# Kernel optimization log

Hardware: AMD Instinct MI355X
Metric: run time of the kernel (lower is better)

The kernel has to match this reference:

```python
import jax, jax.numpy as jnp
import numpy as np


def setup_inputs() -> dict:
    key = jax.random.key(0)
    x = jax.random.normal(key, (8192, 4096), dtype=jnp.float32)
    return {"x": x, "p": 64}


def reference(x, p):
    # training-mode path: find top-p indices per row (descending sort, first p)
    # and overwrite those positions with -1000. mask = ones, so mask*x == x.
    _, idx = jax.lax.top_k(x, p)                      # [B, p] int32
    rows = jnp.arange(x.shape[0])[:, None]            # [B, 1]
    out = x.at[rows, idx].set(jnp.float32(-1000.0))
    return out
```

## Files before the change

kernel.cpp:

```cpp
#include <hip/hip_runtime.h>
#include <stdint.h>

#define COLS 4096
#define NEGV (-1000.0f)

__device__ __forceinline__ uint32_t f2key(float f) {
    uint32_t u = __float_as_uint(f);
    return u ^ (uint32_t)(((int32_t)u >> 31) | (int32_t)0x80000000);
}

extern "C" __global__ __launch_bounds__(256, 4)
void intent_dropout_kernel(const float* __restrict__ x,
                           const int* __restrict__ pp,
                           float* __restrict__ out) {
    __shared__ uint32_t s_keys[COLS];
    __shared__ float    s_grpmax[64];
    __shared__ float    s_C;
    __shared__ uint32_t s_cnt;
    __shared__ uint32_t s_Tkey;
    __shared__ uint32_t s_keq;
    __shared__ uint32_t s_eqcnt;
    __shared__ int      s_eqidx[256];

    const int row  = blockIdx.x;
    const int t    = threadIdx.x;
    const int lane = t & 63;
    const uint32_t P = (uint32_t)pp[0];

    const float4* xr = (const float4*)(x + (size_t)row * COLS);
    float4*       orow = (float4*)(out + (size_t)row * COLS);

    float4 v[4];
#pragma unroll
    for (int j = 0; j < 4; ++j) v[j] = xr[t + 256 * j];

    if (t == 0) { s_cnt = 0u; s_eqcnt = 0u; }

#pragma unroll
    for (int j = 0; j < 4; ++j) {
        float m = fmaxf(fmaxf(v[j].x, v[j].y), fmaxf(v[j].z, v[j].w));
#pragma unroll
        for (int d = 1; d < 16; d <<= 1) m = fmaxf(m, __shfl_xor(m, d, 64));
        if ((lane & 15) == 0) s_grpmax[(t >> 4) + 16 * j] = m;
    }
    __syncthreads();
    if (t < 64) {
        float g = s_grpmax[t];
#pragma unroll
        for (int d = 1; d < 64; d <<= 1) g = fminf(g, __shfl_xor(g, d, 64));
        if (t == 0) s_C = g;
    }
    __syncthreads();
    const uint32_t Ckey = f2key(s_C);

#define PUSH(F) do {                                                         \
        uint32_t k_ = f2key(F);                                              \
        bool pred_ = (k_ >= Ckey);                                           \
        unsigned long long m_ = __ballot(pred_);                             \
        if (m_) {                                                            \
            int ldr_ = (int)__builtin_ctzll(m_);                             \
            uint32_t base_ = 0u;                                             \
            if (lane == ldr_) base_ = atomicAdd(&s_cnt, (uint32_t)__popcll(m_)); \
            base_ = (uint32_t)__shfl((int)base_, ldr_, 64);                  \
            if (pred_) {                                                     \
                uint32_t off_ = (uint32_t)__popcll(m_ & ((1ull << lane) - 1ull)); \
                s_keys[base_ + off_] = k_;                                   \
            }                                                                \
        }                                                                    \
    } while (0)

#pragma unroll
    for (int j = 0; j < 4; ++j) {
        PUSH(v[j].x); PUSH(v[j].y); PUSH(v[j].z); PUSH(v[j].w);
    }
    __syncthreads();
    const uint32_t M = s_cnt;

    if (t < 64) {
        uint32_t rem = P, prefix = 0u;
        if (M <= 1024u) {
            uint32_t kk[16];
#pragma unroll
            for (int q = 0; q < 16; ++q) {
                uint32_t slot = (uint32_t)lane + 64u * q;
                kk[q] = (slot < M) ? s_keys[slot] : 0u;
            }
#pragma unroll
            for (int b = 31; b >= 0; --b) {
                uint32_t cand = prefix | (1u << b);
                uint32_t cnt = 0u;
#pragma unroll
                for (int q = 0; q < 16; ++q)
                    cnt += (uint32_t)(((kk[q] ^ cand) >> b) == 0u);
#pragma unroll
                for (int d = 1; d < 64; d <<= 1) cnt += __shfl_xor(cnt, d, 64);
                if (cnt >= rem) prefix = cand; else rem -= cnt;
            }
        } else {
            uint32_t nk = (M + 63u) >> 6;
            for (int b = 31; b >= 0; --b) {
                uint32_t cand = prefix | (1u << b);
                uint32_t cnt = 0u;
                for (uint32_t q = 0; q < nk; ++q) {
                    uint32_t slot = (uint32_t)lane + 64u * q;
                    if (slot < M)
                        cnt += (uint32_t)(((s_keys[slot] ^ cand) >> b) == 0u);
                }
#pragma unroll
                for (int d = 1; d < 64; d <<= 1) cnt += __shfl_xor(cnt, d, 64);
                if (cnt >= rem) prefix = cand; else rem -= cnt;
            }
        }
        if (t == 0) { s_Tkey = prefix; s_keq = rem; }
    }
    __syncthreads();
    const uint32_t Tkey = s_Tkey;
    const uint32_t keq  = s_keq;

#define EQPUSH(F, IDX) do {                                                  \
        if (f2key(F) == Tkey) {                                              \
            uint32_t s_ = atomicAdd(&s_eqcnt, 1u);                           \
            if (s_ < 256u) s_eqidx[s_] = (IDX);                              \
        }                                                                    \
    } while (0)

#pragma unroll
    for (int j = 0; j < 4; ++j) {
        EQPUSH(v[j].x, 4 * t + 1024 * j + 0);
        EQPUSH(v[j].y, 4 * t + 1024 * j + 1);
        EQPUSH(v[j].z, 4 * t + 1024 * j + 2);
        EQPUSH(v[j].w, 4 * t + 1024 * j + 3);
    }
    __syncthreads();
    const uint32_t eqc = s_eqcnt;

#define PROC(F, IDX) do {                                                    \
        uint32_t k_ = f2key(F);                                              \
        if (k_ > Tkey) { F = NEGV; }                                         \
        else if (k_ == Tkey) {                                               \
            int myi_ = (IDX);                                                \
            uint32_t r_ = 0u;                                                \
            uint32_t n_ = (eqc < 256u) ? eqc : 256u;                         \
            for (uint32_t e = 0; e < n_; ++e)                                \
                r_ += (uint32_t)(s_eqidx[e] < myi_);                         \
            if (r_ < keq) F = NEGV;                                          \
        }                                                                    \
    } while (0)

#pragma unroll
    for (int j = 0; j < 4; ++j) {
        float4 o = v[j];
        PROC(o.x, 4 * t + 1024 * j + 0);
        PROC(o.y, 4 * t + 1024 * j + 1);
        PROC(o.z, 4 * t + 1024 * j + 2);
        PROC(o.w, 4 * t + 1024 * j + 3);
        orow[t + 256 * j] = o;
    }
}

extern "C" void kernel_launch(void* const* d_in, const int* in_sizes, int n_in,
                              void* d_out, int out_size, void* d_ws, size_t ws_size,
                              hipStream_t stream) {
    const float* x  = (const float*)d_in[0];
    const int*   pp = (const int*)d_in[1];
    float*       out = (float*)d_out;
    int rows = in_sizes[0] / COLS;
    hipLaunchKernelGGL(intent_dropout_kernel, dim3(rows), dim3(256), 0, stream,
                       x, pp, out);
}
```

Measured before the change: 250.4 us.

## Replace single-wave bitwise radix select with block-wide 3-pass histogram select

Replaces the 32-iteration bitwise radix search run by one wave over compacted candidate keys with a three-pass shared-memory histogram select (11/11/10 bits) that all 256 threads take part in, using block-wide scans to find the target bin. Keys are kept in registers instead of the original floats, and shared memory shrinks from a 16KB key buffer to two 8KB histograms, so launch bounds rise to 8 blocks per CU for higher occupancy. In exchange it adds histogram zeroing, atomics and several extra barriers per row.

```diff
diff --git a/kernel.cpp b/kernel.cpp
--- a/kernel.cpp
+++ b/kernel.cpp
@@ -8,152 +8,158 @@
     uint32_t u = __float_as_uint(f);
     return u ^ (uint32_t)(((int32_t)u >> 31) | (int32_t)0x80000000);
 }
+__device__ __forceinline__ float key2f(uint32_t k) {
+    uint32_t u = (k & 0x80000000u) ? (k ^ 0x80000000u) : ~k;
+    return __uint_as_float(u);
+}
 
-extern "C" __global__ __launch_bounds__(256, 4)
+template <int PER>
+__device__ __forceinline__ void find_bin(const uint32_t* hist, int t, int lane, int wave,
+                                         uint32_t rem, uint32_t* s_wsum,
+                                         volatile uint32_t* s_dig, volatile uint32_t* s_rem) {
+    const int base = t * PER;
+    uint32_t own[PER];
+    uint32_t L = 0;
+#pragma unroll
+    for (int i = 0; i < PER; ++i) { own[i] = hist[base + i]; L += own[i]; }
+    uint32_t inc = L;
+#pragma unroll
+    for (int d = 1; d < 64; d <<= 1) {
+        uint32_t tmp = (uint32_t)__shfl_down((int)inc, d, 64);
+        if (lane + d < 64) inc += tmp;
+    }
+    if (lane == 0) s_wsum[wave] = inc;
+    __syncthreads();
+    uint32_t U = inc - L;
+#pragma unroll
+    for (int w = 1; w < 4; ++w) if (wave + w < 4) U += s_wsum[wave + w];
+    uint32_t acc = U;
+#pragma unroll
+    for (int i = PER - 1; i >= 0; --i) {
+        uint32_t h = own[i];
+        if (h != 0u && acc < rem && rem <= acc + h) {
+            *s_dig = (uint32_t)(base + i);
+            *s_rem = rem - acc;
+        }
+        acc += h;
+    }
+    __syncthreads();
+}
+
+extern "C" __global__ __launch_bounds__(256, 8)
 void intent_dropout_kernel(const float* __restrict__ x,
                            const int* __restrict__ pp,
                            float* __restrict__ out) {
-    __shared__ uint32_t s_keys[COLS];
-    __shared__ float    s_grpmax[64];
-    __shared__ float    s_C;
-    __shared__ uint32_t s_cnt;
-    __shared__ uint32_t s_Tkey;
-    __shared__ uint32_t s_keq;
+    __shared__ uint32_t s_h1[2048];
+    __shared__ uint32_t s_h2[2048];
+    __shared__ uint32_t s_grpmax[64];
+    __shared__ uint32_t s_wsum[4];
+    __shared__ uint32_t s_Ckey;
+    __shared__ uint32_t s_dig, s_remv;
     __shared__ uint32_t s_eqcnt;
-    __shared__ int      s_eqidx[256];
 
     const int row  = blockIdx.x;
     const int t    = threadIdx.x;
     const int lane = t & 63;
+    const int wave = t >> 6;
     const uint32_t P = (uint32_t)pp[0];
 
-    const float4* xr = (const float4*)(x + (size_t)row * COLS);
+    const float4* xr   = (const float4*)(x + (size_t)row * COLS);
     float4*       orow = (float4*)(out + (size_t)row * COLS);
 
-    float4 v[4];
+    uint32_t keys[16];
 #pragma unroll
-    for (int j = 0; j < 4; ++j) v[j] = xr[t + 256 * j];
-
-    if (t == 0) { s_cnt = 0u; s_eqcnt = 0u; }
+    for (int j = 0; j < 4; ++j) {
+        float4 v = xr[t + 256 * j];
+        keys[4 * j + 0] = f2key(v.x);
+        keys[4 * j + 1] = f2key(v.y);
+        keys[4 * j + 2] = f2key(v.z);
+        keys[4 * j + 3] = f2key(v.w);
+    }
+#pragma unroll
+    for (int i = 0; i < 8; ++i) { s_h1[t + 256 * i] = 0u; s_h2[t + 256 * i] = 0u; }
+    if (t == 0) s_eqcnt = 0u;
 
 #pragma unroll
     for (int j = 0; j < 4; ++j) {
-        float m = fmaxf(fmaxf(v[j].x, v[j].y), fmaxf(v[j].z, v[j].w));
+        uint32_t m = max(max(keys[4 * j], keys[4 * j + 1]), max(keys[4 * j + 2], keys[4 * j + 3]));
 #pragma unroll
-        for (int d = 1; d < 16; d <<= 1) m = fmaxf(m, __shfl_xor(m, d, 64));
+        for (int d = 1; d < 16; d <<= 1) m = max(m, (uint32_t)__shfl_xor((int)m, d, 64));
         if ((lane & 15) == 0) s_grpmax[(t >> 4) + 16 * j] = m;
     }
     __syncthreads();
+
     if (t < 64) {
-        float g = s_grpmax[t];
+        uint32_t g = s_grpmax[t];
 #pragma unroll
-        for (int d = 1; d < 64; d <<= 1) g = fminf(g, __shfl_xor(g, d, 64));
-        if (t == 0) s_C = g;
+        for (int d = 1; d < 64; d <<= 1) g = min(g, (uint32_t)__shfl_xor((int)g, d, 64));
+        if (t == 0) s_Ckey = g;
     }
     __syncthreads();
-    const uint32_t Ckey = f2key(s_C);
+    const uint32_t Ckey = s_Ckey;
 
-#define PUSH(F) do {                                                         \
-        uint32_t k_ = f2key(F);                                              \
-        bool pred_ = (k_ >= Ckey);                                           \
-        unsigned long long m_ = __ballot(pred_);                             \
-        if (m_) {                                                            \
-            int ldr_ = (int)__builtin_ctzll(m_);                             \
-            uint32_t base_ = 0u;                                             \
-            if (lane == ldr_) base_ = atomicAdd(&s_cnt, (uint32_t)__popcll(m_)); \
-            base_ = (uint32_t)__shfl((int)base_, ldr_, 64);                  \
-            if (pred_) {                                                     \
-                uint32_t off_ = (uint32_t)__popcll(m_ & ((1ull << lane) - 1ull)); \
-                s_keys[base_ + off_] = k_;                                   \
-            }                                                                \
-        }                                                                    \
-    } while (0)
+#pragma unroll
+    for (int i = 0; i < 16; ++i)
+        if (keys[i] >= Ckey) atomicAdd(&s_h1[keys[i] >> 21], 1u);
+    __syncthreads();
+    find_bin<8>(s_h1, t, lane, wave, P, s_wsum, &s_dig, &s_remv);
+    const uint32_t d1   = s_dig;
+    const uint32_t rem1 = s_remv;
+
+#pragma unroll
+    for (int i = 0; i < 4; ++i) s_h1[t + 256 * i] = 0u;
+#pragma unroll
+    for (int i = 0; i < 16; ++i)
+        if (keys[i] >= Ckey && (keys[i] >> 21) == d1)
+            atomicAdd(&s_h2[(keys[i] >> 10) & 0x7FFu], 1u);
+    __syncthreads();
+    find_bin<8>(s_h2, t, lane, wave, rem1, s_wsum, &s_dig, &s_remv);
+    const uint32_t d2   = s_dig;
+    const uint32_t rem2 = s_remv;
+    const uint32_t pre21 = (d1 << 11) | d2;
+
+#pragma unroll
+    for (int i = 0; i < 16; ++i)
+        if (keys[i] >= Ckey && (keys[i] >> 10) == pre21)
+            atomicAdd(&s_h1[keys[i] & 0x3FFu], 1u);
+    __syncthreads();
+    find_bin<4>(s_h1, t, lane, wave, rem2, s_wsum, &s_dig, &s_remv);
+    const uint32_t Tkey = (pre21 << 10) | s_dig;
+    const uint32_t keq  = s_remv;
 
 #pragma unroll
     for (int j = 0; j < 4; ++j) {
-        PUSH(v[j].x); PUSH(v[j].y); PUSH(v[j].z); PUSH(v[j].w);
+#pragma unroll
+        for (int c = 0; c < 4; ++c) {
+            if (keys[4 * j + c] == Tkey) {
+                uint32_t s = atomicAdd(&s_eqcnt, 1u);
+                if (s < 2048u) s_h2[s] = (uint32_t)(4 * t + 1024 * j + c);
+            }
+        }
     }
     __syncthreads();
-    const uint32_t M = s_cnt;
-
-    if (t < 64) {
-        uint32_t rem = P, prefix = 0u;
-        if (M <= 1024u) {
-            uint32_t kk[16];
-#pragma unroll
-            for (int q = 0; q < 16; ++q) {
-                uint32_t slot = (uint32_t)lane + 64u * q;
-                kk[q] = (slot < M) ? s_keys[slot] : 0u;
-            }
-#pragma unroll
-            for (int b = 31; b >= 0; --b) {
-                uint32_t cand = prefix | (1u << b);
-                uint32_t cnt = 0u;
-#pragma unroll
-                for (int q = 0; q < 16; ++q)
-                    cnt += (uint32_t)(((kk[q] ^ cand) >> b) == 0u);
-#pragma unroll
-                for (int d = 1; d < 64; d <<= 1) cnt += __shfl_xor(cnt, d, 64);
-                if (cnt >= rem) prefix = cand; else rem -= cnt;
-            }
-        } else {
-            uint32_t nk = (M + 63u) >> 6;
-            for (int b = 31; b >= 0; --b) {
-                uint32_t cand = prefix | (1u << b);
-                uint32_t cnt = 0u;
-                for (uint32_t q = 0; q < nk; ++q) {
-                    uint32_t slot = (uint32_t)lane + 64u * q;
-                    if (slot < M)
-                        cnt += (uint32_t)(((s_keys[slot] ^ cand) >> b) == 0u);
-                }
-#pragma unroll
-                for (int d = 1; d < 64; d <<= 1) cnt += __shfl_xor(cnt, d, 64);
-                if (cnt >= rem) prefix = cand; else rem -= cnt;
-            }
-        }
-        if (t == 0) { s_Tkey = prefix; s_keq = rem; }
-    }
-    __syncthreads();
-    const uint32_t Tkey = s_Tkey;
-    const uint32_t keq  = s_keq;
-
-#define EQPUSH(F, IDX) do {                                                  \
-        if (f2key(F) == Tkey) {                                              \
-            uint32_t s_ = atomicAdd(&s_eqcnt, 1u);                           \
-            if (s_ < 256u) s_eqidx[s_] = (IDX);                              \
-        }                                                                    \
-    } while (0)
+    const uint32_t eqc = (s_eqcnt < 2048u) ? s_eqcnt : 2048u;
 
 #pragma unroll
     for (int j = 0; j < 4; ++j) {
-        EQPUSH(v[j].x, 4 * t + 1024 * j + 0);
-        EQPUSH(v[j].y, 4 * t + 1024 * j + 1);
-        EQPUSH(v[j].z, 4 * t + 1024 * j + 2);
-        EQPUSH(v[j].w, 4 * t + 1024 * j + 3);
-    }
-    __syncthreads();
-    const uint32_t eqc = s_eqcnt;
-
-#define PROC(F, IDX) do {                                                    \
-        uint32_t k_ = f2key(F);                                              \
-        if (k_ > Tkey) { F = NEGV; }                                         \
-        else if (k_ == Tkey) {                                               \
-            int myi_ = (IDX);                                                \
-            uint32_t r_ = 0u;                                                \
-            uint32_t n_ = (eqc < 256u) ? eqc : 256u;                         \
-            for (uint32_t e = 0; e < n_; ++e)                                \
-                r_ += (uint32_t)(s_eqidx[e] < myi_);                         \
-            if (r_ < keq) F = NEGV;                                          \
-        }                                                                    \
-    } while (0)
-
+        float4 o;
+        float* comp = (float*)&o;
 #pragma unroll
-    for (int j = 0; j < 4; ++j) {
-        float4 o = v[j];
-        PROC(o.x, 4 * t + 1024 * j + 0);
-        PROC(o.y, 4 * t + 1024 * j + 1);
-        PROC(o.z, 4 * t + 1024 * j + 2);
-        PROC(o.w, 4 * t + 1024 * j + 3);
+        for (int c = 0; c < 4; ++c) {
+            uint32_t k = keys[4 * j + c];
+            float f;
+            if (k > Tkey) {
+                f = NEGV;
+            } else if (k == Tkey) {
+                uint32_t myi = (uint32_t)(4 * t + 1024 * j + c);
+                uint32_t r = 0;
+                for (uint32_t e = 0; e < eqc; ++e) r += (uint32_t)(s_h2[e] < myi);
+                f = (r < keq) ? NEGV : key2f(k);
+            } else {
+                f = key2f(k);
+            }
+            comp[c] = f;
+        }
         orow[t + 256 * j] = o;
     }
 }
@@ -161,8 +167,8 @@
 extern "C" void kernel_launch(void* const* d_in, const int* in_sizes, int n_in,
                               void* d_out, int out_size, void* d_ws, size_t ws_size,
                               hipStream_t stream) {
-    const float* x  = (const float*)d_in[0];
-    const int*   pp = (const int*)d_in[1];
+    const float* x   = (const float*)d_in[0];
+    const int*   pp  = (const int*)d_in[1];
     float*       out = (float*)d_out;
     int rows = in_sizes[0] / COLS;
     hipLaunchKernelGGL(intent_dropout_kernel, dim3(rows), dim3(256), 0, stream,
```

Result: faster. 231.0 us (-7.7%).
